# Optimization experiments

Measured on AMD Instinct MI355X. Metric: run time of the kernel, lower is better.

Reference implementation:

```python
import jax, jax.numpy as jnp
import numpy as np

B, N_NODES, VOCAB, H = 128, 1023, 2048, 256  # depth-9 perfect binary trees (heap layout)


def setup_inputs() -> dict:
    key = jax.random.key(0)
    k1, k2, k3, k4, k5 = jax.random.split(key, 5)
    tokens = jax.random.randint(k1, (B, N_NODES), 0, VOCAB)
    emb = jax.random.normal(k2, (VOCAB, H), dtype=jnp.float32) * 0.02
    Wx = jax.random.normal(k3, (H, 5 * H), dtype=jnp.float32) * 0.02
    Ul = jax.random.normal(k4, (H, 5 * H), dtype=jnp.float32) * 0.02
    Ur = jax.random.normal(k5, (H, 5 * H), dtype=jnp.float32) * 0.02
    b = jnp.zeros((5 * H,), dtype=jnp.float32)
    return {"tokens": tokens, "emb": emb, "Wx": Wx, "Ul": Ul, "Ur": Ur, "b": b}


def _tree_lstm(tokens, emb, Wx, Ul, Ur, b):
    # tokens: [B, 2^(D+1)-1] in level-order heap layout; children of heap index i
    # are 2i+1, 2i+2 -> within level d+1 they sit at offsets 2k, 2k+1.
    n_nodes = tokens.shape[1]
    depth = int(np.log2(n_nodes + 1)) - 1
    hdim = emb.shape[1]
    x_all = emb[tokens]  # [B, N, H] embedding lookup (memory-bound gather)
    h = c = None
    for d in range(depth, -1, -1):  # bottom-up over levels (fixed structural loop)
        start, n = 2 ** d - 1, 2 ** d
        x = x_all[:, start:start + n]  # [B, n, H]
        gates = jnp.einsum('bnh,hg->bng', x, Wx) + b
        if h is not None:
            hl, hr = h[:, 0::2], h[:, 1::2]
            cl, cr = c[:, 0::2], c[:, 1::2]
            gates = gates + jnp.einsum('bnh,hg->bng', hl, Ul) + jnp.einsum('bnh,hg->bng', hr, Ur)
        i, fl, fr, o, u = jnp.split(gates, 5, axis=-1)
        i, fl, fr, o = map(jax.nn.sigmoid, (i, fl, fr, o))
        u = jnp.tanh(u)
        c_new = i * u
        if c is not None:
            c_new = c_new + fl * cl + fr * cr
        c = c_new
        h = o * jnp.tanh(c)
    return h[:, 0], c[:, 0]  # root states, each [B, H]


def reference(tokens, emb, Wx, Ul, Ur, b):
    h_root, _ = _tree_lstm(tokens, emb, Wx, Ul, Ur, b)
    return h_root  # [B, H]
```

## Files before the change

kernel.cpp:

```cpp
#include <hip/hip_runtime.h>
#include <hip/hip_bf16.h>
#include <math.h>

#define B_SZ   128
#define HDIM   256
#define NG     1280
#define NNODES 1023
#define VOCAB  2048

typedef unsigned int uint32;
typedef short  short8v  __attribute__((ext_vector_type(8)));
typedef float  float4v  __attribute__((ext_vector_type(4)));

__device__ __forceinline__ float sigm(float x) {
    return 1.0f / (1.0f + __expf(-x));
}
__device__ __forceinline__ float tanh_fast(float x) {
    return 2.0f / (1.0f + __expf(-2.0f * x)) - 1.0f;
}
__device__ __forceinline__ float bf2f(unsigned short u) {
    return __uint_as_float(((uint32)u) << 16);
}
__device__ __forceinline__ unsigned short f2bf(float f) {
    uint32 x = __float_as_uint(f);
    uint32 r = (x + 0x7FFFu + ((x >> 16) & 1u)) >> 16;
    return (unsigned short)r;
}

__device__ __forceinline__ void dma16(const unsigned short* gptr, unsigned short* lptr) {
    __builtin_amdgcn_global_load_lds(
        (const __attribute__((address_space(1))) void*)gptr,
        (__attribute__((address_space(3))) void*)lptr, 16, 0, 0);
}

__global__ __launch_bounds__(256) void embb_kernel(
    const float* __restrict__ emb, unsigned short* __restrict__ embb)
{
    const int t = blockIdx.x * 256 + threadIdx.x;
    const float4 v0 = *(const float4*)(emb + (size_t)t * 8);
    const float4 v1 = *(const float4*)(emb + (size_t)t * 8 + 4);
    short8v o;
    o[0] = (short)f2bf(v0.x); o[1] = (short)f2bf(v0.y);
    o[2] = (short)f2bf(v0.z); o[3] = (short)f2bf(v0.w);
    o[4] = (short)f2bf(v1.x); o[5] = (short)f2bf(v1.y);
    o[6] = (short)f2bf(v1.z); o[7] = (short)f2bf(v1.w);
    *(short8v*)(embb + (size_t)t * 8) = o;
}

__global__ __launch_bounds__(256) void prep_wtf(
    const float* __restrict__ Ul, const float* __restrict__ Ur,
    const float* __restrict__ Wx, unsigned short* __restrict__ WTf)
{
    const int t = blockIdx.x * 256 + threadIdx.x;
    const int l = t & 63;
    const int q = l >> 4, c = l & 15;
    const int ks = (t >> 6) % 24;
    const int ng = t / (24 * 64);
    const int col = ng * 16 + c;
    const int k = ks * 32 + q * 8;
    const float* src = (k < 256) ? (Ul + (size_t)k * NG + col)
                     : (k < 512) ? (Ur + (size_t)(k - 256) * NG + col)
                                 : (Wx + (size_t)(k - 512) * NG + col);
    short8v v;
    #pragma unroll
    for (int j = 0; j < 8; ++j) v[j] = (short)f2bf(src[(size_t)j * NG]);
    *(short8v*)(WTf + (size_t)t * 8) = v;
}

__global__ __launch_bounds__(256, 2) void ewb_mfma(
    const unsigned short* __restrict__ WTf, const unsigned short* __restrict__ embb,
    const float* __restrict__ bias, unsigned short* __restrict__ EWb)
{
    __shared__ __align__(16) unsigned short Ab[2][4096];
    __shared__ __align__(16) unsigned short wbE[20480];

    const int tid  = threadIdx.x;
    const int lane = tid & 63;
    const int w    = tid >> 6;
    const int quad = lane >> 4, col15 = lane & 15;
    const int jt = blockIdx.x;
    const int rowBase = blockIdx.y * 64;
    const int jbase   = jt * 64;

    const unsigned short* agp[2];
    unsigned short* ldst[2];
    #pragma unroll
    for (int t = 0; t < 2; ++t) {
        const int ch = 2 * w + t, sub = ch >> 2, rt = ch & 3;
        const int srow = rowBase + rt * 16 + col15;
        agp[t]  = embb + (size_t)srow * HDIM + sub * 32 + quad * 8;
        ldst[t] = &Ab[0][0] + ch * 512;
    }

    const short8v* WTfv = (const short8v*)WTf;
    uint32 boff[5];
    #pragma unroll
    for (int g = 0; g < 5; ++g)
        boff[g] = ((g * 16 + jt * 4 + w) * 24 + 16) * 64 + lane;

    float4v acc[4][5];
    #pragma unroll
    for (int rt = 0; rt < 4; ++rt)
        #pragma unroll
        for (int g = 0; g < 5; ++g)
            #pragma unroll
            for (int e = 0; e < 4; ++e) acc[rt][g][e] = 0.0f;

    dma16(agp[0], ldst[0]); dma16(agp[1], ldst[1]);
    __syncthreads();

    #pragma unroll
    for (int s = 0; s < 4; ++s) {
        if (s < 3) {
            dma16(agp[0] + (s + 1) * 64, ldst[0] + ((s + 1) & 1) * 4096);
            dma16(agp[1] + (s + 1) * 64, ldst[1] + ((s + 1) & 1) * 4096);
        }
        #pragma unroll
        for (int sub = 0; sub < 2; ++sub) {
            short8v bf[5];
            #pragma unroll
            for (int g = 0; g < 5; ++g) bf[g] = WTfv[boff[g] + (s * 2 + sub) * 64];
            #pragma unroll
            for (int rt = 0; rt < 4; ++rt) {
                const short8v af = *(const short8v*)&Ab[s & 1][(sub * 4 + rt) * 512 + lane * 8];
                #pragma unroll
                for (int g = 0; g < 5; ++g)
                    acc[rt][g] = __builtin_amdgcn_mfma_f32_16x16x32_bf16(
                        af, bf[g], acc[rt][g], 0, 0, 0);
            }
        }
        __syncthreads();
    }

    const int jl = w * 16 + col15;
    const int j  = jbase + jl;
    float bz[5];
    #pragma unroll
    for (int g = 0; g < 5; ++g) bz[g] = bias[g * 256 + j];
    const int jchunk = jl >> 3, jpos = jl & 7;

    #pragma unroll
    for (int rt = 0; rt < 4; ++rt) {
        #pragma unroll
        for (int reg = 0; reg < 4; ++reg) {
            const int rr = rt * 16 + quad * 4 + reg;
            const int roff = ((jchunk + 2 * quad) & 7) * 8 + jpos;
            #pragma unroll
            for (int g = 0; g < 5; ++g)
                wbE[(g * 64 + rr) * 64 + roff] = f2bf(acc[rt][g][reg] + bz[g]);
        }
    }
    __syncthreads();

    #pragma unroll
    for (int k2 = 0; k2 < 10; ++k2) {
        const int c = tid + k2 * 256;
        const int g = c >> 9, rr = (c >> 3) & 63, u = c & 7;
        const int ru = (u + 2 * ((rr >> 2) & 3)) & 7;
        const short8v v = *(const short8v*)&wbE[(g * 64 + rr) * 64 + ru * 8];
        *(short8v*)(EWb + (size_t)(rowBase + rr) * NG + g * 256 + jbase + u * 8) = v;
    }
}

__global__ __launch_bounds__(256) void leaftab_kernel(
    const unsigned short* __restrict__ EWb,
    unsigned short* __restrict__ Hleaf, unsigned short* __restrict__ Cleaf)
{
    const int t = blockIdx.x * 256 + threadIdx.x;
    const int tok = t >> 8, j = t & 255;
    const float gi = bf2f(EWb[(size_t)tok * NG + j]);
    const float go = bf2f(EWb[(size_t)tok * NG + 768 + j]);
    const float gu = bf2f(EWb[(size_t)tok * NG + 1024 + j]);
    const float c = sigm(gi) * tanh_fast(gu);
    const float h = sigm(go) * tanh_fast(c);
    Hleaf[t] = f2bf(h);
    Cleaf[t] = f2bf(c);
}

__global__ __launch_bounds__(256, 2) void level_kernel(
    const unsigned short* __restrict__ WTf, const int* __restrict__ tokens,
    const unsigned short* __restrict__ embb,
    const unsigned short* __restrict__ Hleaf, const unsigned short* __restrict__ Cleaf,
    const unsigned short* __restrict__ hsrc, const unsigned short* __restrict__ csrc,
    const float* __restrict__ bias,
    unsigned short* __restrict__ hdst, unsigned short* __restrict__ cdst,
    float* __restrict__ out, const int d)
{
    const int n = 1 << d;

    __shared__ __align__(16) unsigned short Ab[2][4096];

    const int tid  = threadIdx.x;
    const int lane = tid & 63;
    const int w    = tid >> 6;
    const int quad = lane >> 4, col15 = lane & 15;
    const int jt = blockIdx.x;
    const int rowBase = blockIdx.y * 64;
    const int jbase   = jt * 64;

    const unsigned short* agp_lo[2];
    const unsigned short* agp_hi[2];
    const unsigned short* agp_x[2];
    unsigned short* ldst[2];
    #pragma unroll
    for (int t = 0; t < 2; ++t) {
        const int ch = 2 * w + t, sub = ch >> 2, rt = ch & 3;
        const int srow = rowBase + rt * 16 + col15;
        const int b = srow >> d, i = srow & (n - 1);
        const int tokN = tokens[b * NNODES + (n - 1) + i];
        agp_x[t] = embb + (size_t)tokN * HDIM + sub * 32 + quad * 8;
        if (d == 8) {
            const int tokL = tokens[b * NNODES + 511 + 2 * i];
            const int tokR = tokens[b * NNODES + 512 + 2 * i];
            agp_lo[t] = Hleaf + (size_t)tokL * HDIM + sub * 32 + quad * 8;
            agp_hi[t] = Hleaf + (size_t)tokR * HDIM + sub * 32 + quad * 8;
        } else {
            agp_lo[t] = hsrc + (size_t)(2 * srow) * HDIM + sub * 32 + quad * 8;
            agp_hi[t] = agp_lo[t] + HDIM;
        }
        ldst[t] = &Ab[0][0] + ch * 512;
    }

    const short8v* WTfv = (const short8v*)WTf;
    uint32 boff[5];
    #pragma unroll
    for (int g = 0; g < 5; ++g)
        boff[g] = ((g * 16 + jt * 4 + w) * 24) * 64 + lane;

    const int jl = w * 16 + col15;
    const int j  = jbase + jl;
    float bz[5];
    #pragma unroll
    for (int g = 0; g < 5; ++g) bz[g] = bias[g * 256 + j];

    float4v acc[4][5];
    #pragma unroll
    for (int rt = 0; rt < 4; ++rt)
        #pragma unroll
        for (int g = 0; g < 5; ++g)
            #pragma unroll
            for (int e = 0; e < 4; ++e) acc[rt][g][e] = 0.0f;

    dma16(agp_lo[0], ldst[0]); dma16(agp_lo[1], ldst[1]);
    __syncthreads();

    #pragma unroll
    for (int s = 0; s < 12; ++s) {
        if (s < 11) {
            const int sn = s + 1;
            #pragma unroll
            for (int t = 0; t < 2; ++t) {
                const unsigned short* p = (sn < 4) ? (agp_lo[t] + sn * 64)
                                        : (sn < 8) ? (agp_hi[t] + (sn - 4) * 64)
                                                   : (agp_x[t]  + (sn - 8) * 64);
                dma16(p, ldst[t] + (sn & 1) * 4096);
            }
        }

        #pragma unroll
        for (int sub = 0; sub < 2; ++sub) {
            short8v bf[5];
            #pragma unroll
            for (int g = 0; g < 5; ++g) bf[g] = WTfv[boff[g] + (s * 2 + sub) * 64];
            #pragma unroll
            for (int rt = 0; rt < 4; ++rt) {
                const short8v af = *(const short8v*)&Ab[s & 1][(sub * 4 + rt) * 512 + lane * 8];
                #pragma unroll
                for (int g = 0; g < 5; ++g)
                    acc[rt][g] = __builtin_amdgcn_mfma_f32_16x16x32_bf16(
                        af, bf[g], acc[rt][g], 0, 0, 0);
            }
        }
        __syncthreads();
    }

    float hv[4][4], cv[4][4];
    #pragma unroll
    for (int rt = 0; rt < 4; ++rt) {
        #pragma unroll
        for (int reg = 0; reg < 4; ++reg) {
            const int rr = rt * 16 + quad * 4 + reg;
            const int grow = rowBase + rr;
            float cl, cr;
            if (d == 8) {
                const int b = grow >> 8, i = grow & 255;
                const int tokL = tokens[b * NNODES + 511 + 2 * i];
                const int tokR = tokens[b * NNODES + 512 + 2 * i];
                cl = bf2f(Cleaf[(size_t)tokL * HDIM + j]);
                cr = bf2f(Cleaf[(size_t)tokR * HDIM + j]);
            } else {
                cl = bf2f(csrc[(size_t)(2 * grow) * HDIM + j]);
                cr = bf2f(csrc[(size_t)(2 * grow + 1) * HDIM + j]);
            }
            const float gi  = acc[rt][0][reg] + bz[0];
            const float gfl = acc[rt][1][reg] + bz[1];
            const float gfr = acc[rt][2][reg] + bz[2];
            const float go  = acc[rt][3][reg] + bz[3];
            const float gu  = acc[rt][4][reg] + bz[4];
            const float ii = sigm(gi), fl = sigm(gfl), fr = sigm(gfr), oo = sigm(go);
            const float uu = tanh_fast(gu);
            const float c = ii * uu + fl * cl + fr * cr;
            const float h = oo * tanh_fast(c);
            cv[rt][reg] = c; hv[rt][reg] = h;
            if (d == 0) out[(size_t)grow * HDIM + j] = h;
        }
    }
    if (d == 0) return;

    unsigned short* wb = &Ab[0][0];
    const int jchunk = jl >> 3, jpos = jl & 7;
    #pragma unroll
    for (int rt = 0; rt < 4; ++rt) {
        #pragma unroll
        for (int reg = 0; reg < 4; ++reg) {
            const int rr = rt * 16 + quad * 4 + reg;
            const int roff = ((jchunk + 2 * quad) & 7) * 8 + jpos;
            wb[rr * 64 + roff]        = f2bf(hv[rt][reg]);
            wb[4096 + rr * 64 + roff] = f2bf(cv[rt][reg]);
        }
    }
    __syncthreads();
    #pragma unroll
    for (int k2 = 0; k2 < 4; ++k2) {
        const int c = tid + k2 * 256;
        const int arr = c >> 9, rr = (c >> 3) & 63, u = c & 7;
        const int ru = (u + 2 * ((rr >> 2) & 3)) & 7;
        const short8v v = *(const short8v*)(wb + (arr * 4096 + rr * 64 + ru * 8));
        unsigned short* dstp = (arr ? cdst : hdst) +
            (size_t)(rowBase + rr) * HDIM + jbase + u * 8;
        *(short8v*)dstp = v;
    }
}

extern "C" void kernel_launch(void* const* d_in, const int* in_sizes, int n_in,
                              void* d_out, int out_size, void* d_ws, size_t ws_size,
                              hipStream_t stream)
{
    const int*   tokens = (const int*)d_in[0];
    const float* emb    = (const float*)d_in[1];
    const float* Wx     = (const float*)d_in[2];
    const float* Ul     = (const float*)d_in[3];
    const float* Ur     = (const float*)d_in[4];
    const float* bias   = (const float*)d_in[5];
    float* out = (float*)d_out;

    const size_t EW_ELEMS  = (size_t)VOCAB * NG;
    const size_t EMB_ELEMS = (size_t)VOCAB * HDIM;
    const size_t WTF_ELEMS = (size_t)80 * 24 * 64 * 8;
    const size_t LT_ELEMS  = (size_t)VOCAB * HDIM;
    const size_t SLOT_A    = (size_t)16384 * HDIM;
    const size_t SLOT_B    = (size_t)32768 * HDIM;
    const size_t REQUIRED  = (EW_ELEMS + EMB_ELEMS + WTF_ELEMS + 2 * LT_ELEMS
                              + 2 * (SLOT_A + SLOT_B)) * 2;
    if (ws_size < REQUIRED || d_ws == nullptr) return;

    char* ws = (char*)d_ws;
    unsigned short* EWb   = (unsigned short*)ws;
    unsigned short* embb  = EWb + EW_ELEMS;
    unsigned short* WTf   = embb + EMB_ELEMS;
    unsigned short* Hleaf = WTf + WTF_ELEMS;
    unsigned short* Cleaf = Hleaf + LT_ELEMS;
    unsigned short* hA    = Cleaf + LT_ELEMS;
    unsigned short* cA    = hA + SLOT_A;
    unsigned short* hB    = cA + SLOT_A;
    unsigned short* cB    = hB + SLOT_B;

    embb_kernel<<<dim3(256), 256, 0, stream>>>(emb, embb);
    prep_wtf<<<dim3(480), 256, 0, stream>>>(Ul, Ur, Wx, WTf);
    ewb_mfma<<<dim3(4, 32), 256, 0, stream>>>(WTf, embb, bias, EWb);
    leaftab_kernel<<<dim3(2048), 256, 0, stream>>>(EWb, Hleaf, Cleaf);

    for (int d = 8; d >= 0; --d) {
        const int NRB = 2 << d;
        const bool evenD = ((d & 1) == 0);
        const unsigned short* hs = evenD ? hA : hB;
        const unsigned short* cs = evenD ? cA : cB;
        unsigned short* hd = evenD ? hB : hA;
        unsigned short* cd = evenD ? cB : cA;
        level_kernel<<<dim3(4, NRB), 256, 0, stream>>>(
            WTf, tokens, embb, Hleaf, Cleaf, hs, cs, bias, hd, cd, out, d);
    }
}
```

Baseline: 378.3 us.

## Double LDS stage depth to halve pipeline steps and template leaf level

Each pipeline stage now loads 128 K-elements per row (four 16-byte DMAs per thread into a larger 2x8192 LDS buffer), so the K loop runs 6 stages instead of 12 and needs half as many barriers. Source addresses become 32-bit byte offsets instead of pointer arrays, which should cut register use. The kernel is templated on the leaf level so the d==8 branches are resolved at compile time. The trade-off is double the LDS per block (32 KB), which could limit occupancy, plus more outstanding DMAs per stage.

Result: faster. 356.6 us (-5.7%).

```diff
diff --git a/kernel.cpp b/kernel.cpp
--- a/kernel.cpp
+++ b/kernel.cpp
@@ -177,6 +177,7 @@
     Cleaf[t] = f2bf(c);
 }
 
+template <bool LEAF>
 __global__ __launch_bounds__(256, 2) void level_kernel(
     const unsigned short* __restrict__ WTf, const int* __restrict__ tokens,
     const unsigned short* __restrict__ embb,
@@ -188,7 +189,7 @@
 {
     const int n = 1 << d;
 
-    __shared__ __align__(16) unsigned short Ab[2][4096];
+    __shared__ __align__(16) unsigned short Ab[2][8192];
 
     const int tid  = threadIdx.x;
     const int lane = tid & 63;
@@ -198,28 +199,23 @@
     const int rowBase = blockIdx.y * 64;
     const int jbase   = jt * 64;
 
-    const unsigned short* agp_lo[2];
-    const unsigned short* agp_hi[2];
-    const unsigned short* agp_x[2];
-    unsigned short* ldst[2];
-    #pragma unroll
-    for (int t = 0; t < 2; ++t) {
-        const int ch = 2 * w + t, sub = ch >> 2, rt = ch & 3;
-        const int srow = rowBase + rt * 16 + col15;
+    const uint32 inrow = (uint32)(w * 64 + quad * 16);
+    uint32 oL[4], oR[4], oN[4];
+    #pragma unroll
+    for (int t = 0; t < 4; ++t) {
+        const int srow = rowBase + t * 16 + col15;
         const int b = srow >> d, i = srow & (n - 1);
-        const int tokN = tokens[b * NNODES + (n - 1) + i];
-        agp_x[t] = embb + (size_t)tokN * HDIM + sub * 32 + quad * 8;
-        if (d == 8) {
-            const int tokL = tokens[b * NNODES + 511 + 2 * i];
-            const int tokR = tokens[b * NNODES + 512 + 2 * i];
-            agp_lo[t] = Hleaf + (size_t)tokL * HDIM + sub * 32 + quad * 8;
-            agp_hi[t] = Hleaf + (size_t)tokR * HDIM + sub * 32 + quad * 8;
+        oN[t] = (uint32)tokens[b * NNODES + (n - 1) + i] * 512u + inrow;
+        if (LEAF) {
+            oL[t] = (uint32)tokens[b * NNODES + 511 + 2 * i] * 512u + inrow;
+            oR[t] = (uint32)tokens[b * NNODES + 512 + 2 * i] * 512u + inrow;
         } else {
-            agp_lo[t] = hsrc + (size_t)(2 * srow) * HDIM + sub * 32 + quad * 8;
-            agp_hi[t] = agp_lo[t] + HDIM;
-        }
-        ldst[t] = &Ab[0][0] + ch * 512;
-    }
+            oL[t] = (uint32)(2 * srow) * 512u + inrow;
+            oR[t] = oL[t] + 512u;
+        }
+    }
+    const char* hb = LEAF ? (const char*)Hleaf : (const char*)hsrc;
+    const char* xb = (const char*)embb;
 
     const short8v* WTfv = (const short8v*)WTf;
     uint32 boff[5];
@@ -241,27 +237,33 @@
             #pragma unroll
             for (int e = 0; e < 4; ++e) acc[rt][g][e] = 0.0f;
 
-    dma16(agp_lo[0], ldst[0]); dma16(agp_lo[1], ldst[1]);
+    {
+        unsigned short* dst = &Ab[0][0] + w * 2048;
+        #pragma unroll
+        for (int t = 0; t < 4; ++t)
+            dma16((const unsigned short*)(hb + oL[t]), dst + t * 512);
+    }
     __syncthreads();
 
     #pragma unroll
-    for (int s = 0; s < 12; ++s) {
-        if (s < 11) {
+    for (int s = 0; s < 6; ++s) {
+        if (s < 5) {
             const int sn = s + 1;
-            #pragma unroll
-            for (int t = 0; t < 2; ++t) {
-                const unsigned short* p = (sn < 4) ? (agp_lo[t] + sn * 64)
-                                        : (sn < 8) ? (agp_hi[t] + (sn - 4) * 64)
-                                                   : (agp_x[t]  + (sn - 8) * 64);
-                dma16(p, ldst[t] + (sn & 1) * 4096);
+            unsigned short* dst = &Ab[sn & 1][0] + w * 2048;
+            #pragma unroll
+            for (int t = 0; t < 4; ++t) {
+                const char* p = (sn < 2) ? (hb + oL[t] + sn * 256)
+                              : (sn < 4) ? (hb + oR[t] + (sn - 2) * 256)
+                                         : (xb + oN[t] + (sn - 4) * 256);
+                dma16((const unsigned short*)p, dst + t * 512);
             }
         }
 
         #pragma unroll
-        for (int sub = 0; sub < 2; ++sub) {
+        for (int sub = 0; sub < 4; ++sub) {
             short8v bf[5];
             #pragma unroll
-            for (int g = 0; g < 5; ++g) bf[g] = WTfv[boff[g] + (s * 2 + sub) * 64];
+            for (int g = 0; g < 5; ++g) bf[g] = WTfv[boff[g] + (s * 4 + sub) * 64];
             #pragma unroll
             for (int rt = 0; rt < 4; ++rt) {
                 const short8v af = *(const short8v*)&Ab[s & 1][(sub * 4 + rt) * 512 + lane * 8];
@@ -282,7 +284,7 @@
             const int rr = rt * 16 + quad * 4 + reg;
             const int grow = rowBase + rr;
             float cl, cr;
-            if (d == 8) {
+            if (LEAF) {
                 const int b = grow >> 8, i = grow & 255;
                 const int tokL = tokens[b * NNODES + 511 + 2 * i];
                 const int tokR = tokens[b * NNODES + 512 + 2 * i];
@@ -302,10 +304,10 @@
             const float c = ii * uu + fl * cl + fr * cr;
             const float h = oo * tanh_fast(c);
             cv[rt][reg] = c; hv[rt][reg] = h;
-            if (d == 0) out[(size_t)grow * HDIM + j] = h;
-        }
-    }
-    if (d == 0) return;
+            if (!LEAF && d == 0) out[(size_t)grow * HDIM + j] = h;
+        }
+    }
+    if (!LEAF && d == 0) return;
 
     unsigned short* wb = &Ab[0][0];
     const int jchunk = jl >> 3, jpos = jl & 7;
@@ -377,7 +379,12 @@
         const unsigned short* cs = evenD ? cA : cB;
         unsigned short* hd = evenD ? hB : hA;
         unsigned short* cd = evenD ? cB : cA;
-        level_kernel<<<dim3(4, NRB), 256, 0, stream>>>(
-            WTf, tokens, embb, Hleaf, Cleaf, hs, cs, bias, hd, cd, out, d);
-    }
-}
+        if (d == 8) {
+            level_kernel<true><<<dim3(4, NRB), 256, 0, stream>>>(
+                WTf, tokens, embb, Hleaf, Cleaf, hs, cs, bias, hd, cd, out, d);
+        } else {
+            level_kernel<false><<<dim3(4, NRB), 256, 0, stream>>>(
+                WTf, tokens, embb, Hleaf, Cleaf, hs, cs, bias, hd, cd, out, d);
+        }
+    }
+}
```
